# Kernel tuning notes

Measured on AMD Instinct MI355X. Metric: run time of the kernel, lower is better.

Reference implementation:

```python
import jax, jax.numpy as jnp
import numpy as np

MARGIN = 0.3
N, D = 4096, 512
NUM_CLASSES = 64

def setup_inputs() -> dict:
    key = jax.random.key(0)
    k1, k2, k3 = jax.random.split(key, 3)
    src_feat = jax.random.normal(k1, (N, D), dtype=jnp.float32)
    tgt_feat = jax.random.normal(k2, (N, D), dtype=jnp.float32)
    labels = jax.random.randint(k3, (N,), 0, NUM_CLASSES, dtype=jnp.int64)
    return {"src_feat": src_feat, "tgt_feat": tgt_feat, "labels": labels}

def reference(src_feat, tgt_feat, labels):
    # squared Euclidean distance matrix [n, n]
    e1 = jnp.sum(src_feat * src_feat, axis=1, keepdims=True)   # [n,1]
    e2 = jnp.sum(tgt_feat * tgt_feat, axis=1, keepdims=True).T  # [1,n]
    dist = e1 + e2 - 2.0 * (src_feat @ tgt_feat.T)
    dist = jnp.maximum(dist, 0.0)  # matches dist_mat[dist_mat < 0] = 0
    # same-label mask [n, n]
    mask = labels[:, None] == labels[None, :]
    # hard positive: max dist among same-label cols; hard negative: min among others
    dist_ap = jnp.max(jnp.where(mask, dist, -jnp.inf), axis=1)  # [n]
    dist_an = jnp.min(jnp.where(mask, jnp.inf, dist), axis=1)   # [n]
    # MarginRankingLoss with target y = 1: mean(relu(-(an - ap) + margin))
    loss = jnp.mean(jax.nn.relu(dist_ap - dist_an + MARGIN))
    return loss
```

## Files before the change

kernel.cpp:

```cpp
#include <hip/hip_runtime.h>
#include <hip/hip_bf16.h>
#include <stdint.h>

#define N_PTS 4096
#define DIM 512
#define MARGIN_F 0.3f
#define POS_INF_BITS 0x7f800000

typedef short bf16x8 __attribute__((ext_vector_type(8)));
typedef float f32x4 __attribute__((ext_vector_type(4)));

__device__ __forceinline__ unsigned short f2bf(float f) {
    unsigned int b = __float_as_uint(f);
    b += 0x7FFF + ((b >> 16) & 1);
    return (unsigned short)(b >> 16);
}

__device__ __forceinline__ void async16(const unsigned short* g, unsigned short* l) {
    __builtin_amdgcn_global_load_lds(
        (const __attribute__((address_space(1))) unsigned int*)g,
        (__attribute__((address_space(3))) unsigned int*)l,
        16, 0, 0);
}

__global__ __launch_bounds__(256) void prep_kernel(
    const float* __restrict__ src, const float* __restrict__ tgt,
    unsigned short* __restrict__ src_bf, unsigned short* __restrict__ tgt_bf,
    float* __restrict__ e1, float* __restrict__ e2,
    float* __restrict__ ap, float* __restrict__ an)
{
    const int row  = blockIdx.x * 4 + (threadIdx.x >> 6);
    const int lane = threadIdx.x & 63;

    const float4* s4 = (const float4*)(src + (size_t)row * DIM);
    const float4* t4 = (const float4*)(tgt + (size_t)row * DIM);
    float4 a0 = s4[lane], a1 = s4[lane + 64];
    float4 b0 = t4[lane], b1 = t4[lane + 64];

    ushort4 u;
    ushort4* so = (ushort4*)(src_bf + (size_t)row * DIM);
    ushort4* to = (ushort4*)(tgt_bf + (size_t)row * DIM);
    u.x = f2bf(a0.x); u.y = f2bf(a0.y); u.z = f2bf(a0.z); u.w = f2bf(a0.w); so[lane] = u;
    u.x = f2bf(a1.x); u.y = f2bf(a1.y); u.z = f2bf(a1.z); u.w = f2bf(a1.w); so[lane + 64] = u;
    u.x = f2bf(b0.x); u.y = f2bf(b0.y); u.z = f2bf(b0.z); u.w = f2bf(b0.w); to[lane] = u;
    u.x = f2bf(b1.x); u.y = f2bf(b1.y); u.z = f2bf(b1.z); u.w = f2bf(b1.w); to[lane + 64] = u;

    float s1 = a0.x*a0.x + a0.y*a0.y + a0.z*a0.z + a0.w*a0.w
             + a1.x*a1.x + a1.y*a1.y + a1.z*a1.z + a1.w*a1.w;
    float s2 = b0.x*b0.x + b0.y*b0.y + b0.z*b0.z + b0.w*b0.w
             + b1.x*b1.x + b1.y*b1.y + b1.z*b1.z + b1.w*b1.w;
    for (int off = 32; off; off >>= 1) {
        s1 += __shfl_down(s1, off);
        s2 += __shfl_down(s2, off);
    }
    if (lane == 0) {
        e1[row] = s1;
        e2[row] = s2;
        ap[row] = 0.0f;
        an[row] = __int_as_float(POS_INF_BITS);
    }
}

#define BM 128
#define BN 128
#define BK 32

__global__ __launch_bounds__(256) void dist_kernel(
    const unsigned short* __restrict__ src_bf,
    const unsigned short* __restrict__ tgt_bf,
    const float* __restrict__ e1, const float* __restrict__ e2,
    const int* __restrict__ labels,
    float* __restrict__ ap, float* __restrict__ an)
{
    __shared__ unsigned short As[BM * BK];
    __shared__ unsigned short Bs[BN * BK];
    __shared__ int   li[BM];
    __shared__ int   lj[BN];
    __shared__ float e1s[BM];
    __shared__ float e2s[BN];

    const int i0 = blockIdx.y * BM;
    const int j0 = blockIdx.x * BN;
    const int t = threadIdx.x;
    const int lane = t & 63;
    const int wave = t >> 6;

    if (t < BM)      { li[t] = labels[i0 + t]; e1s[t] = e1[i0 + t]; }
    else             { int u = t - BM; lj[u] = labels[j0 + u]; e2s[u] = e2[j0 + u]; }

    const unsigned short* gA0 = src_bf + (size_t)(i0 + (t >> 2)) * DIM + (t & 3) * 8;
    const unsigned short* gA1 = src_bf + (size_t)(i0 + 64 + (t >> 2)) * DIM + (t & 3) * 8;
    const unsigned short* gB0 = tgt_bf + (size_t)(j0 + (t >> 2)) * DIM + (t & 3) * 8;
    const unsigned short* gB1 = tgt_bf + (size_t)(j0 + 64 + (t >> 2)) * DIM + (t & 3) * 8;
    unsigned short* lds0 = &As[0] + wave * 512;
    unsigned short* lds1 = &As[0] + 2048 + wave * 512;
    unsigned short* ldsB0 = &Bs[0] + wave * 512;
    unsigned short* ldsB1 = &Bs[0] + 2048 + wave * 512;

    const int wm = (wave >> 1) * 64;
    const int wn = (wave & 1) * 64;
    const int fr = lane & 15;
    const int quad = lane >> 4;

    f32x4 acc[4][4];
    #pragma unroll
    for (int a = 0; a < 4; a++)
        #pragma unroll
        for (int b = 0; b < 4; b++)
            acc[a][b] = (f32x4){0.f, 0.f, 0.f, 0.f};

    for (int kk = 0; kk < DIM; kk += BK) {
        __syncthreads();
        async16(gA0 + kk, lds0);
        async16(gA1 + kk, lds1);
        async16(gB0 + kk, ldsB0);
        async16(gB1 + kk, ldsB1);
        __syncthreads();

        bf16x8 af[4], bf[4];
        #pragma unroll
        for (int x = 0; x < 4; x++) {
            af[x] = *(const bf16x8*)&As[(wm + x * 16 + fr) * BK + quad * 8];
            bf[x] = *(const bf16x8*)&Bs[(wn + x * 16 + fr) * BK + quad * 8];
        }
        #pragma unroll
        for (int tm = 0; tm < 4; tm++)
            #pragma unroll
            for (int tn = 0; tn < 4; tn++)
                acc[tm][tn] = __builtin_amdgcn_mfma_f32_16x16x32_bf16(
                    af[tm], bf[tn], acc[tm][tn], 0, 0, 0);
    }

    const float INF = __int_as_float(POS_INF_BITS);
    #pragma unroll
    for (int tm = 0; tm < 4; tm++) {
        #pragma unroll
        for (int r = 0; r < 4; r++) {
            const int rl = wm + tm * 16 + quad * 4 + r;
            const float e1v = e1s[rl];
            const int   liv = li[rl];
            float apv = 0.0f;
            float anv = INF;
            #pragma unroll
            for (int tn = 0; tn < 4; tn++) {
                const int cl = wn + tn * 16 + fr;
                float d = e1v + e2s[cl] - 2.0f * acc[tm][tn][r];
                d = fmaxf(d, 0.0f);
                if (liv == lj[cl]) apv = fmaxf(apv, d);
                else               anv = fminf(anv, d);
            }
            #pragma unroll
            for (int off = 1; off < 16; off <<= 1) {
                apv = fmaxf(apv, __shfl_xor(apv, off));
                anv = fminf(anv, __shfl_xor(anv, off));
            }
            if (fr == 0) {
                atomicMax((int*)&ap[i0 + rl], __float_as_int(apv));
                atomicMin((int*)&an[i0 + rl], __float_as_int(anv));
            }
        }
    }
}

__global__ __launch_bounds__(256) void loss_kernel(
    const float* __restrict__ ap, const float* __restrict__ an,
    float* __restrict__ out)
{
    const int t = threadIdx.x;
    float s = 0.0f;
    for (int i = t; i < N_PTS; i += 256) {
        float v = ap[i] - an[i] + MARGIN_F;
        s += fmaxf(v, 0.0f);
    }
    for (int off = 32; off; off >>= 1) s += __shfl_down(s, off);
    __shared__ float red[4];
    if ((t & 63) == 0) red[t >> 6] = s;
    __syncthreads();
    if (t == 0) out[0] = (red[0] + red[1] + red[2] + red[3]) / (float)N_PTS;
}

extern "C" void kernel_launch(void* const* d_in, const int* in_sizes, int n_in,
                              void* d_out, int out_size, void* d_ws, size_t ws_size,
                              hipStream_t stream) {
    const float* src   = (const float*)d_in[0];
    const float* tgt   = (const float*)d_in[1];
    const int* labels  = (const int*)d_in[2];

    char* ws = (char*)d_ws;
    const size_t featB = (size_t)N_PTS * DIM * sizeof(unsigned short);
    unsigned short* src_bf = (unsigned short*)ws;
    unsigned short* tgt_bf = (unsigned short*)(ws + featB);
    float* e1 = (float*)(ws + 2 * featB);
    float* e2 = e1 + N_PTS;
    float* ap = e2 + N_PTS;
    float* an = ap + N_PTS;

    prep_kernel<<<N_PTS / 4, 256, 0, stream>>>(src, tgt, src_bf, tgt_bf, e1, e2, ap, an);
    dim3 grid(N_PTS / BN, N_PTS / BM);
    dist_kernel<<<grid, 256, 0, stream>>>(src_bf, tgt_bf, e1, e2, labels, ap, an);
    loss_kernel<<<1, 256, 0, stream>>>(ap, an, (float*)d_out);
}
```

Before: 109.2 us.

## Fuse loss reduction into dist kernel; widen BK with XOR-swizzled LDS tiles

Removes the separate loss kernel. The last dist block, found with an atomic completion counter that prep_kernel resets, now performs the final mean reduction. The K tile doubles to 64 so there are half as many sync/load rounds. LDS columns are XOR-swizzled to avoid bank conflicts on the fragment reads. A launch-bounds occupancy hint is added. This saves one kernel launch and halves the barriers, at the cost of more LDS per block and a serialized tail in the last block.

New measurement: 141.6 us. +29.7%, slower.

```diff
diff --git a/kernel.cpp b/kernel.cpp
--- a/kernel.cpp
+++ b/kernel.cpp
@@ -27,10 +27,13 @@
     const float* __restrict__ src, const float* __restrict__ tgt,
     unsigned short* __restrict__ src_bf, unsigned short* __restrict__ tgt_bf,
     float* __restrict__ e1, float* __restrict__ e2,
-    float* __restrict__ ap, float* __restrict__ an)
+    float* __restrict__ ap, float* __restrict__ an,
+    int* __restrict__ done_ctr)
 {
     const int row  = blockIdx.x * 4 + (threadIdx.x >> 6);
     const int lane = threadIdx.x & 63;
+
+    if (blockIdx.x == 0 && threadIdx.x == 0) *done_ctr = 0;
 
     const float4* s4 = (const float4*)(src + (size_t)row * DIM);
     const float4* t4 = (const float4*)(tgt + (size_t)row * DIM);
@@ -63,14 +66,16 @@
 
 #define BM 128
 #define BN 128
-#define BK 32
-
-__global__ __launch_bounds__(256) void dist_kernel(
+#define BK 64
+#define NBLK 1024
+
+__global__ __launch_bounds__(256, 4) void dist_kernel(
     const unsigned short* __restrict__ src_bf,
     const unsigned short* __restrict__ tgt_bf,
     const float* __restrict__ e1, const float* __restrict__ e2,
     const int* __restrict__ labels,
-    float* __restrict__ ap, float* __restrict__ an)
+    float* __restrict__ ap, float* __restrict__ an,
+    int* __restrict__ done_ctr, float* __restrict__ out)
 {
     __shared__ unsigned short As[BM * BK];
     __shared__ unsigned short Bs[BN * BK];
@@ -78,6 +83,7 @@
     __shared__ int   lj[BN];
     __shared__ float e1s[BM];
     __shared__ float e2s[BN];
+    __shared__ int   is_last;
 
     const int i0 = blockIdx.y * BM;
     const int j0 = blockIdx.x * BN;
@@ -85,22 +91,21 @@
     const int lane = t & 63;
     const int wave = t >> 6;
 
-    if (t < BM)      { li[t] = labels[i0 + t]; e1s[t] = e1[i0 + t]; }
-    else             { int u = t - BM; lj[u] = labels[j0 + u]; e2s[u] = e2[j0 + u]; }
-
-    const unsigned short* gA0 = src_bf + (size_t)(i0 + (t >> 2)) * DIM + (t & 3) * 8;
-    const unsigned short* gA1 = src_bf + (size_t)(i0 + 64 + (t >> 2)) * DIM + (t & 3) * 8;
-    const unsigned short* gB0 = tgt_bf + (size_t)(j0 + (t >> 2)) * DIM + (t & 3) * 8;
-    const unsigned short* gB1 = tgt_bf + (size_t)(j0 + 64 + (t >> 2)) * DIM + (t & 3) * 8;
-    unsigned short* lds0 = &As[0] + wave * 512;
-    unsigned short* lds1 = &As[0] + 2048 + wave * 512;
-    unsigned short* ldsB0 = &Bs[0] + wave * 512;
-    unsigned short* ldsB1 = &Bs[0] + 2048 + wave * 512;
+    if (t < BM) { li[t] = labels[i0 + t]; e1s[t] = e1[i0 + t]; }
+    else        { int u = t - BM; lj[u] = labels[j0 + u]; e2s[u] = e2[j0 + u]; }
+
+    const int srow = t >> 3;
+    const int scol = ((t & 7) ^ (srow & 7)) * 8;
+    const unsigned short* gA = src_bf + (size_t)(i0 + srow) * DIM + scol;
+    const unsigned short* gB = tgt_bf + (size_t)(j0 + srow) * DIM + scol;
+    unsigned short* ldsA = &As[0] + wave * 512;
+    unsigned short* ldsB = &Bs[0] + wave * 512;
 
     const int wm = (wave >> 1) * 64;
     const int wn = (wave & 1) * 64;
     const int fr = lane & 15;
     const int quad = lane >> 4;
+    const int fsw = fr & 7;
 
     f32x4 acc[4][4];
     #pragma unroll
@@ -111,24 +116,31 @@
 
     for (int kk = 0; kk < DIM; kk += BK) {
         __syncthreads();
-        async16(gA0 + kk, lds0);
-        async16(gA1 + kk, lds1);
-        async16(gB0 + kk, ldsB0);
-        async16(gB1 + kk, ldsB1);
+        #pragma unroll
+        for (int g = 0; g < 4; g++) {
+            async16(gA + (size_t)g * 32 * DIM + kk, ldsA + g * 2048);
+            async16(gB + (size_t)g * 32 * DIM + kk, ldsB + g * 2048);
+        }
         __syncthreads();
 
-        bf16x8 af[4], bf[4];
-        #pragma unroll
-        for (int x = 0; x < 4; x++) {
-            af[x] = *(const bf16x8*)&As[(wm + x * 16 + fr) * BK + quad * 8];
-            bf[x] = *(const bf16x8*)&Bs[(wn + x * 16 + fr) * BK + quad * 8];
-        }
-        #pragma unroll
-        for (int tm = 0; tm < 4; tm++)
-            #pragma unroll
-            for (int tn = 0; tn < 4; tn++)
-                acc[tm][tn] = __builtin_amdgcn_mfma_f32_16x16x32_bf16(
-                    af[tm], bf[tn], acc[tm][tn], 0, 0, 0);
+        #pragma unroll
+        for (int s = 0; s < 2; s++) {
+            bf16x8 af[4], bf[4];
+            #pragma unroll
+            for (int x = 0; x < 4; x++) {
+                const int ar = wm + x * 16 + fr;
+                const int br = wn + x * 16 + fr;
+                const int cp = ((s << 2) | quad) ^ fsw;
+                af[x] = *(const bf16x8*)&As[ar * BK + cp * 8];
+                bf[x] = *(const bf16x8*)&Bs[br * BK + cp * 8];
+            }
+            #pragma unroll
+            for (int tm = 0; tm < 4; tm++)
+                #pragma unroll
+                for (int tn = 0; tn < 4; tn++)
+                    acc[tm][tn] = __builtin_amdgcn_mfma_f32_16x16x32_bf16(
+                        af[tm], bf[tn], acc[tm][tn], 0, 0, 0);
+        }
     }
 
     const float INF = __int_as_float(POS_INF_BITS);
@@ -160,23 +172,32 @@
             }
         }
     }
-}
-
-__global__ __launch_bounds__(256) void loss_kernel(
-    const float* __restrict__ ap, const float* __restrict__ an,
-    float* __restrict__ out)
-{
-    const int t = threadIdx.x;
-    float s = 0.0f;
-    for (int i = t; i < N_PTS; i += 256) {
-        float v = ap[i] - an[i] + MARGIN_F;
-        s += fmaxf(v, 0.0f);
-    }
-    for (int off = 32; off; off >>= 1) s += __shfl_down(s, off);
-    __shared__ float red[4];
-    if ((t & 63) == 0) red[t >> 6] = s;
+
     __syncthreads();
-    if (t == 0) out[0] = (red[0] + red[1] + red[2] + red[3]) / (float)N_PTS;
+    if (t == 0) {
+        __threadfence();
+        int old = __hip_atomic_fetch_add(done_ctr, 1, __ATOMIC_ACQ_REL,
+                                         __HIP_MEMORY_SCOPE_AGENT);
+        is_last = (old == NBLK - 1);
+    }
+    __syncthreads();
+    if (is_last) {
+        __threadfence();
+        float s = 0.0f;
+        for (int i = t; i < N_PTS; i += 256) {
+            int ai = __hip_atomic_load((int*)&ap[i], __ATOMIC_RELAXED,
+                                       __HIP_MEMORY_SCOPE_AGENT);
+            int ni = __hip_atomic_load((int*)&an[i], __ATOMIC_RELAXED,
+                                       __HIP_MEMORY_SCOPE_AGENT);
+            float v = __int_as_float(ai) - __int_as_float(ni) + MARGIN_F;
+            s += fmaxf(v, 0.0f);
+        }
+        for (int off = 32; off; off >>= 1) s += __shfl_down(s, off);
+        __shared__ float red[4];
+        if ((t & 63) == 0) red[t >> 6] = s;
+        __syncthreads();
+        if (t == 0) out[0] = (red[0] + red[1] + red[2] + red[3]) / (float)N_PTS;
+    }
 }
 
 extern "C" void kernel_launch(void* const* d_in, const int* in_sizes, int n_in,
@@ -194,9 +215,11 @@
     float* e2 = e1 + N_PTS;
     float* ap = e2 + N_PTS;
     float* an = ap + N_PTS;
-
-    prep_kernel<<<N_PTS / 4, 256, 0, stream>>>(src, tgt, src_bf, tgt_bf, e1, e2, ap, an);
+    int* done_ctr = (int*)(an + N_PTS);
+
+    prep_kernel<<<N_PTS / 4, 256, 0, stream>>>(src, tgt, src_bf, tgt_bf,
+                                               e1, e2, ap, an, done_ctr);
     dim3 grid(N_PTS / BN, N_PTS / BM);
-    dist_kernel<<<grid, 256, 0, stream>>>(src_bf, tgt_bf, e1, e2, labels, ap, an);
-    loss_kernel<<<1, 256, 0, stream>>>(ap, an, (float*)d_out);
-}
+    dist_kernel<<<grid, 256, 0, stream>>>(src_bf, tgt_bf, e1, e2, labels,
+                                          ap, an, done_ctr, (float*)d_out);
+}
```
